# Kernel optimization log

Hardware: AMD Instinct MI355X
Metric: run time of the kernel (lower is better)

Reference implementation:

```python
import jax, jax.numpy as jnp
import numpy as np

NH = 16  # num_attention_heads
HD = 64  # attention_head_size (hidden 1024 / 16)

def _gelu(x):
    # matches torch.jit gelu: x * 0.5 * (1 + erf(x / 1.41421))
    return x * 0.5 * (1.0 + jax.lax.erf(x / 1.41421))

def setup_inputs() -> dict:
    key = jax.random.key(0)
    ks = jax.random.split(key, 6)
    B, S, H = 32, 512, 1024
    sc = 1.0 / np.sqrt(H)
    return {
        "hidden_states": jax.random.normal(ks[0], (B, S, H), jnp.float32),
        "Wq": jax.random.normal(ks[1], (H, H), jnp.float32) * sc,
        "bq": jnp.zeros((H,), jnp.float32),
        "Wk": jax.random.normal(ks[2], (H, H), jnp.float32) * sc,
        "bk": jnp.zeros((H,), jnp.float32),
        "Wv": jax.random.normal(ks[3], (H, H), jnp.float32) * sc,
        "bv": jnp.zeros((H,), jnp.float32),
        "Wp": jax.random.normal(ks[4], (3 * S, S), jnp.float32) * (1.0 / np.sqrt(3 * S)),
        "bp": jnp.zeros((S,), jnp.float32),
    }

def reference(hidden_states, Wq, bq, Wk, bk, Wv, bv, Wp, bp):
    b, s, h = hidden_states.shape
    # transpose_for_scores in the original is a pure .view (reshape), not a permute
    q = (hidden_states @ Wq + bq).reshape(b, NH, s, HD)
    k = (hidden_states @ Wk + bk).reshape(b, NH, s, HD)
    v = (hidden_states @ Wv + bv).reshape(b, NH, s, HD)
    # pooled global value: Linear over the (3*seq) axis, then gelu
    qkv = jnp.concatenate([q, k, v], axis=-2)              # (b, nh, 3s, hd)
    gv = jnp.swapaxes(qkv, -1, -2) @ Wp + bp               # (b, nh, hd, s)
    gv = _gelu(jnp.swapaxes(gv, -1, -2))                   # (b, nh, s, hd)
    # einsum('bnij,bnji->bni', q, k^T) == per-position dot product
    local = jnp.sum(q * k, axis=-1, keepdims=True)         # (b, nh, s, 1)
    scores = jnp.concatenate([local, jnp.zeros_like(local)], axis=-1)
    scores = scores / np.sqrt(HD)                          # (b, nh, s, 2)
    probs = jax.nn.softmax(scores, axis=-1)                # dropout prob = 0 (eval)
    v2 = jnp.stack([v, gv], axis=-2)                       # (b, nh, s, 2, hd)
    ctx = jnp.einsum('bnsk,bnskd->bnsd', probs, v2)        # (b, nh, s, hd)
    ctx = jnp.transpose(ctx, (0, 2, 1, 3)).reshape(b, s, NH * HD)
    return ctx
```

## Files before the change

### kernel.cpp

```cpp
#include <hip/hip_runtime.h>


typedef unsigned short ushort_t;
typedef __attribute__((ext_vector_type(8))) short short8;
typedef __attribute__((ext_vector_type(8))) unsigned short ushort8;
typedef __attribute__((ext_vector_type(4))) float f32x4;

#define ASYNC16(gp, lp) __builtin_amdgcn_global_load_lds( \
    (const __attribute__((address_space(1))) void*)(gp),  \
    (__attribute__((address_space(3))) void*)(lp), 16, 0, 0)

__device__ __forceinline__ ushort_t f2b(float f) {
  union { float f; unsigned int u; } v; v.f = f;
  unsigned int r = v.u + 0x7FFFu + ((v.u >> 16) & 1u);
  return (ushort_t)(r >> 16);
}
__device__ __forceinline__ float b2f(ushort_t b) {
  union { unsigned int u; float f; } v; v.u = ((unsigned int)b) << 16;
  return v.f;
}

#define OFF_HSB 0ull
#define OFF_WQT (33554432ull)
#define OFF_WKT (OFF_WQT + 2097152ull)
#define OFF_WVT (OFF_WKT + 2097152ull)
#define OFF_WPT (OFF_WVT + 2097152ull)
#define OFF_QF  (OFF_WPT + 1572864ull)
#define OFF_KF  (OFF_QF + 33554432ull)
#define OFF_VF  (OFF_KF + 33554432ull)

extern "C" __global__ __launch_bounds__(256) void k_cast(
    const float* __restrict__ src, ushort_t* __restrict__ dst) {
  int i = blockIdx.x * 256 + threadIdx.x;
  const float4* s = (const float4*)src + (size_t)i * 2;
  float4 a = s[0], b = s[1];
  ushort8 o;
  o[0] = f2b(a.x); o[1] = f2b(a.y); o[2] = f2b(a.z); o[3] = f2b(a.w);
  o[4] = f2b(b.x); o[5] = f2b(b.y); o[6] = f2b(b.z); o[7] = f2b(b.w);
  *((ushort8*)dst + i) = o;
}

extern "C" __global__ __launch_bounds__(256) void k_wt(
    const float* __restrict__ s0, const float* __restrict__ s1,
    const float* __restrict__ s2, const float* __restrict__ s3,
    ushort_t* __restrict__ d0, ushort_t* __restrict__ d1,
    ushort_t* __restrict__ d2, ushort_t* __restrict__ d3) {
  int z = blockIdx.z;
  const float* src = (z == 0) ? s0 : (z == 1) ? s1 : (z == 2) ? s2 : s3;
  ushort_t* dst    = (z == 0) ? d0 : (z == 1) ? d1 : (z == 2) ? d2 : d3;
  int R = (z == 3) ? 1536 : 1024;
  int C = (z == 3) ? 512  : 1024;
  int c0 = blockIdx.x * 64, r0 = blockIdx.y * 64;
  if (c0 >= C || r0 >= R) return;
  __shared__ ushort_t tl[64][80];
  int t = threadIdx.x;
  {
    int lr = t >> 2, cg = (t & 3) * 16;
    const float* sp = src + (size_t)(r0 + lr) * C + c0 + cg;
    #pragma unroll
    for (int i = 0; i < 16; ++i) tl[lr][cg + i] = f2b(sp[i]);
  }
  __syncthreads();
  {
    int lc = t >> 2, rg = (t & 3) * 16;
    ushort_t* dp = dst + (size_t)(c0 + lc) * R + r0 + rg;
    #pragma unroll
    for (int i = 0; i < 16; ++i) dp[i] = tl[rg + i][lc];
  }
}

extern "C" __global__ __launch_bounds__(256) void k_qkv(
    const ushort_t* __restrict__ A,
    const ushort_t* __restrict__ WTq, const ushort_t* __restrict__ WTk, const ushort_t* __restrict__ WTv,
    const float* __restrict__ bq, const float* __restrict__ bk, const float* __restrict__ bv,
    ushort_t* __restrict__ Qf, ushort_t* __restrict__ Kf, ushort_t* __restrict__ Vf) {
  int z = blockIdx.z;
  const ushort_t* WT = (z == 0) ? WTq : (z == 1) ? WTk : WTv;
  const float* bias  = (z == 0) ? bq  : (z == 1) ? bk  : bv;
  ushort_t* out      = (z == 0) ? Qf  : (z == 1) ? Kf  : Vf;

  int glin = blockIdx.y * 8 + blockIdx.x;
  int nl = (glin & 7) * 128 + (glin >> 3);
  int n0 = (nl & 7) * 128, m0 = (nl >> 3) * 128;

  __shared__ ushort_t lA[128 * 32];
  __shared__ ushort_t lB[128 * 32];
  int t = threadIdx.x, lane = t & 63, wave = t >> 6;
  int wr = (wave >> 1) * 64, wc = (wave & 1) * 64;

  f32x4 acc[4][4];
  #pragma unroll
  for (int mi = 0; mi < 4; ++mi)
    #pragma unroll
    for (int ni = 0; ni < 4; ++ni)
      acc[mi][ni] = (f32x4){0.f, 0.f, 0.f, 0.f};

  for (int k0 = 0; k0 < 1024; k0 += 32) {
    #pragma unroll
    for (int j = 0; j < 2; ++j) {
      int u = j * 256 + t;
      ASYNC16(A + (size_t)(m0 + (u >> 2)) * 1024 + k0 + (u & 3) * 8,
              (char*)lA + (j * 256 + wave * 64) * 16);
    }
    #pragma unroll
    for (int j = 0; j < 2; ++j) {
      int u = j * 256 + t;
      ASYNC16(WT + (size_t)(n0 + (u >> 2)) * 1024 + k0 + (u & 3) * 8,
              (char*)lB + (j * 256 + wave * 64) * 16);
    }
    __syncthreads();
    short8 af[4], bf[4];
    #pragma unroll
    for (int mi = 0; mi < 4; ++mi)
      af[mi] = *(const short8*)&lA[(wr + mi * 16 + (lane & 15)) * 32 + (lane >> 4) * 8];
    #pragma unroll
    for (int ni = 0; ni < 4; ++ni)
      bf[ni] = *(const short8*)&lB[(wc + ni * 16 + (lane & 15)) * 32 + (lane >> 4) * 8];
    #pragma unroll
    for (int mi = 0; mi < 4; ++mi)
      #pragma unroll
      for (int ni = 0; ni < 4; ++ni)
        acc[mi][ni] = __builtin_amdgcn_mfma_f32_16x16x32_bf16(af[mi], bf[ni], acc[mi][ni], 0, 0, 0);
    __syncthreads();
  }
  #pragma unroll
  for (int ni = 0; ni < 4; ++ni) {
    int gc = n0 + wc + ni * 16 + (lane & 15);
    float bv_ = bias[gc];
    #pragma unroll
    for (int mi = 0; mi < 4; ++mi) {
      int gr = m0 + wr + mi * 16 + ((lane >> 4) << 2);
      #pragma unroll
      for (int r = 0; r < 4; ++r)
        out[(size_t)(gr + r) * 1024 + gc] = f2b(acc[mi][ni][r] + bv_);
    }
  }
}

extern "C" __global__ __launch_bounds__(256) void k_tr(
    const ushort_t* __restrict__ src, ushort_t* __restrict__ dst) {
  int bn = blockIdx.x;
  const ushort_t* s = src + (size_t)bn * 32768;
  ushort_t* d = dst + (size_t)bn * 32768;
  __shared__ ushort_t tl[64][80];
  int t = threadIdx.x;
  for (int c = 0; c < 8; ++c) {
    #pragma unroll
    for (int j = 0; j < 2; ++j) {
      int u = j * 256 + t;
      int row = u >> 3, ch = (u & 7) * 8;
      uint4 v = *(const uint4*)&s[(size_t)(c * 64 + row) * 64 + ch];
      const ushort_t* pv = (const ushort_t*)&v;
      #pragma unroll
      for (int i = 0; i < 8; ++i) tl[ch + i][row] = pv[i];
    }
    __syncthreads();
    #pragma unroll
    for (int j = 0; j < 2; ++j) {
      int u = j * 256 + t;
      int dd = u >> 3, ch = (u & 7) * 8;
      *(uint4*)&d[(size_t)dd * 512 + c * 64 + ch] = *(const uint4*)&tl[dd][ch];
    }
    __syncthreads();
  }
}

extern "C" __global__ __launch_bounds__(256) void k_gv(
    const ushort_t* __restrict__ WpT,
    const ushort_t* __restrict__ QT, const ushort_t* __restrict__ KT, const ushort_t* __restrict__ VT,
    const float* __restrict__ bp, float* __restrict__ out) {
  int sh = blockIdx.x;
  int bn = blockIdx.y;
  int b = bn >> 4, nh = bn & 15;
  int s0 = sh * 256;
  int t = threadIdx.x, lane = t & 63, wave = t >> 6;

  __shared__ ushort_t lA[256 * 64];
  __shared__ ushort_t lB[64 * 64];
  __shared__ float p0s[256];

  const ushort_t* QTb = QT + (size_t)bn * 32768;
  const ushort_t* KTb = KT + (size_t)bn * 32768;
  const ushort_t* VTb = VT + (size_t)bn * 32768;

  {
    int s2 = s0 + t;
    float dot = 0.f;
    #pragma unroll 8
    for (int d = 0; d < 64; ++d)
      dot += b2f(QTb[(size_t)d * 512 + s2]) * b2f(KTb[(size_t)d * 512 + s2]);
    p0s[t] = 1.0f / (1.0f + __expf(-dot * 0.125f));
  }

  f32x4 acc[4][4];
  #pragma unroll
  for (int mi = 0; mi < 4; ++mi)
    #pragma unroll
    for (int ni = 0; ni < 4; ++ni)
      acc[mi][ni] = (f32x4){0.f, 0.f, 0.f, 0.f};

  for (int kt = 0; kt < 24; ++kt) {
    int t0 = kt * 64;
    const ushort_t* XT = (t0 < 512) ? QTb : (t0 < 1024) ? KTb : VTb;
    int t0l = t0 & 511;
    #pragma unroll
    for (int j = 0; j < 8; ++j) {
      int u = j * 256 + t;
      ASYNC16(WpT + (size_t)(s0 + (u >> 3)) * 1536 + t0 + (u & 7) * 8,
              (char*)lA + (j * 256 + wave * 64) * 16);
    }
    #pragma unroll
    for (int j = 0; j < 2; ++j) {
      int u = j * 256 + t;
      ASYNC16(XT + (size_t)(u >> 3) * 512 + t0l + (u & 7) * 8,
              (char*)lB + (j * 256 + wave * 64) * 16);
    }
    __syncthreads();
    #pragma unroll
    for (int kk = 0; kk < 2; ++kk) {
      short8 af[4], bf[4];
      #pragma unroll
      for (int mi = 0; mi < 4; ++mi)
        af[mi] = *(const short8*)&lA[(wave * 64 + mi * 16 + (lane & 15)) * 64 + kk * 32 + (lane >> 4) * 8];
      #pragma unroll
      for (int ni = 0; ni < 4; ++ni)
        bf[ni] = *(const short8*)&lB[(ni * 16 + (lane & 15)) * 64 + kk * 32 + (lane >> 4) * 8];
      #pragma unroll
      for (int mi = 0; mi < 4; ++mi)
        #pragma unroll
        for (int ni = 0; ni < 4; ++ni)
          acc[mi][ni] = __builtin_amdgcn_mfma_f32_16x16x32_bf16(af[mi], bf[ni], acc[mi][ni], 0, 0, 0);
    }
    __syncthreads();
  }

  size_t outb = (size_t)b * 512 * 1024 + (size_t)nh * 64;
  #pragma unroll
  for (int mi = 0; mi < 4; ++mi) {
    int sl = wave * 64 + mi * 16 + ((lane >> 4) << 2);
    #pragma unroll
    for (int r = 0; r < 4; ++r) {
      int s2 = s0 + sl + r;
      float p0 = p0s[sl + r];
      float bpv = bp[s2];
      #pragma unroll
      for (int ni = 0; ni < 4; ++ni) {
        int d = ni * 16 + (lane & 15);
        float g = acc[mi][ni][r] + bpv;
        float ge = 0.5f * g * (1.0f + erff(g / 1.41421f));
        float v = b2f(VTb[(size_t)d * 512 + s2]);
        out[outb + (size_t)s2 * 1024 + d] = p0 * v + (1.0f - p0) * ge;
      }
    }
  }
}

extern "C" void kernel_launch(void* const* d_in, const int* in_sizes, int n_in,
                              void* d_out, int out_size, void* d_ws, size_t ws_size,
                              hipStream_t stream) {
  const float* hs = (const float*)d_in[0];
  const float* Wq = (const float*)d_in[1];
  const float* bq = (const float*)d_in[2];
  const float* Wk = (const float*)d_in[3];
  const float* bk = (const float*)d_in[4];
  const float* Wv = (const float*)d_in[5];
  const float* bv = (const float*)d_in[6];
  const float* Wp = (const float*)d_in[7];
  const float* bp = (const float*)d_in[8];

  char* w = (char*)d_ws;
  ushort_t* hsb = (ushort_t*)(w + OFF_HSB);
  ushort_t* WqT = (ushort_t*)(w + OFF_WQT);
  ushort_t* WkT = (ushort_t*)(w + OFF_WKT);
  ushort_t* WvT = (ushort_t*)(w + OFF_WVT);
  ushort_t* WpT = (ushort_t*)(w + OFF_WPT);
  ushort_t* Qf  = (ushort_t*)(w + OFF_QF);
  ushort_t* Kf  = (ushort_t*)(w + OFF_KF);
  ushort_t* Vf  = (ushort_t*)(w + OFF_VF);
  ushort_t* QTt = (ushort_t*)(w + OFF_HSB);
  ushort_t* KTt = (ushort_t*)(w + OFF_QF);
  ushort_t* VTt = (ushort_t*)(w + OFF_KF);

  k_cast<<<8192, 256, 0, stream>>>(hs, hsb);
  k_wt<<<dim3(16, 24, 4), 256, 0, stream>>>(Wq, Wk, Wv, Wp, WqT, WkT, WvT, WpT);
  k_qkv<<<dim3(8, 128, 3), 256, 0, stream>>>(hsb, WqT, WkT, WvT, bq, bk, bv, Qf, Kf, Vf);
  k_tr<<<512, 256, 0, stream>>>(Qf, QTt);
  k_tr<<<512, 256, 0, stream>>>(Kf, KTt);
  k_tr<<<512, 256, 0, stream>>>(Vf, VTt);
  k_gv<<<dim3(2, 512), 256, 0, stream>>>(WpT, QTt, KTt, VTt, bp, (float*)d_out);
}
```

Baseline: 413.1 us.

## Share Wp tile across two batch-heads per block in k_gv

Each k_gv block now handles two (batch, head) pairs, so each Wp tile loaded into LDS feeds both. Waves split by head and by a 128-row half, and each wave accumulates 8x4 MFMA tiles instead of 4x4. This halves the Wp global traffic per output and puts blockIdx.x on the batch-head so neighbouring blocks share Wp. The local q·k dot also switches to vectorized 4-wide loads. The cost is more accumulator registers (launch bounds set to 2 blocks per SM), more LDS and half as many blocks.

```diff
diff --git a/kernel.cpp b/kernel.cpp
--- a/kernel.cpp
+++ b/kernel.cpp
@@ -165,83 +165,98 @@
   }
 }
 
-extern "C" __global__ __launch_bounds__(256) void k_gv(
+extern "C" __global__ __launch_bounds__(256, 2) void k_gv(
     const ushort_t* __restrict__ WpT,
     const ushort_t* __restrict__ QT, const ushort_t* __restrict__ KT, const ushort_t* __restrict__ VT,
     const float* __restrict__ bp, float* __restrict__ out) {
-  int sh = blockIdx.x;
-  int bn = blockIdx.y;
-  int b = bn >> 4, nh = bn & 15;
+  int bng = blockIdx.x;
+  int sh  = blockIdx.y;
   int s0 = sh * 256;
+  int bn0 = bng * 2;
   int t = threadIdx.x, lane = t & 63, wave = t >> 6;
+  int wbn = wave & 1;
+  int wr  = (wave >> 1) * 128;
 
   __shared__ ushort_t lA[256 * 64];
-  __shared__ ushort_t lB[64 * 64];
-  __shared__ float p0s[256];
-
-  const ushort_t* QTb = QT + (size_t)bn * 32768;
-  const ushort_t* KTb = KT + (size_t)bn * 32768;
-  const ushort_t* VTb = VT + (size_t)bn * 32768;
-
-  {
-    int s2 = s0 + t;
-    float dot = 0.f;
+  __shared__ ushort_t lB[2 * 64 * 64];
+  __shared__ float p0s[2][256];
+
+  if (t < 128) {
+    int bnl = t >> 6, qi = t & 63;
+    const ushort_t* Qb = QT + (size_t)(bn0 + bnl) * 32768 + s0 + qi * 4;
+    const ushort_t* Kb = KT + (size_t)(bn0 + bnl) * 32768 + s0 + qi * 4;
+    float dd0 = 0.f, dd1 = 0.f, dd2 = 0.f, dd3 = 0.f;
     #pragma unroll 8
-    for (int d = 0; d < 64; ++d)
-      dot += b2f(QTb[(size_t)d * 512 + s2]) * b2f(KTb[(size_t)d * 512 + s2]);
-    p0s[t] = 1.0f / (1.0f + __expf(-dot * 0.125f));
-  }
-
-  f32x4 acc[4][4];
+    for (int d = 0; d < 64; ++d) {
+      uint2 qv = *(const uint2*)(Qb + (size_t)d * 512);
+      uint2 kv = *(const uint2*)(Kb + (size_t)d * 512);
+      dd0 += b2f(qv.x & 0xffff) * b2f(kv.x & 0xffff);
+      dd1 += b2f(qv.x >> 16)    * b2f(kv.x >> 16);
+      dd2 += b2f(qv.y & 0xffff) * b2f(kv.y & 0xffff);
+      dd3 += b2f(qv.y >> 16)    * b2f(kv.y >> 16);
+    }
+    p0s[bnl][qi * 4 + 0] = 1.0f / (1.0f + __expf(-dd0 * 0.125f));
+    p0s[bnl][qi * 4 + 1] = 1.0f / (1.0f + __expf(-dd1 * 0.125f));
+    p0s[bnl][qi * 4 + 2] = 1.0f / (1.0f + __expf(-dd2 * 0.125f));
+    p0s[bnl][qi * 4 + 3] = 1.0f / (1.0f + __expf(-dd3 * 0.125f));
+  }
+
+  f32x4 acc[8][4];
   #pragma unroll
-  for (int mi = 0; mi < 4; ++mi)
+  for (int mi = 0; mi < 8; ++mi)
     #pragma unroll
     for (int ni = 0; ni < 4; ++ni)
       acc[mi][ni] = (f32x4){0.f, 0.f, 0.f, 0.f};
 
   for (int kt = 0; kt < 24; ++kt) {
     int t0 = kt * 64;
-    const ushort_t* XT = (t0 < 512) ? QTb : (t0 < 1024) ? KTb : VTb;
+    const ushort_t* XT = (t0 < 512) ? QT : (t0 < 1024) ? KT : VT;
     int t0l = t0 & 511;
     #pragma unroll
     for (int j = 0; j < 8; ++j) {
-      int u = j * 256 + t;
-      ASYNC16(WpT + (size_t)(s0 + (u >> 3)) * 1536 + t0 + (u & 7) * 8,
+      int uu = j * 256 + t;
+      ASYNC16(WpT + (size_t)(s0 + (uu >> 3)) * 1536 + t0 + (uu & 7) * 8,
               (char*)lA + (j * 256 + wave * 64) * 16);
     }
     #pragma unroll
-    for (int j = 0; j < 2; ++j) {
-      int u = j * 256 + t;
-      ASYNC16(XT + (size_t)(u >> 3) * 512 + t0l + (u & 7) * 8,
-              (char*)lB + (j * 256 + wave * 64) * 16);
+    for (int bl = 0; bl < 2; ++bl) {
+      const ushort_t* Xb = XT + (size_t)(bn0 + bl) * 32768;
+      #pragma unroll
+      for (int j = 0; j < 2; ++j) {
+        int uu = j * 256 + t;
+        ASYNC16(Xb + (size_t)(uu >> 3) * 512 + t0l + (uu & 7) * 8,
+                (char*)lB + bl * 8192 + (j * 256 + wave * 64) * 16);
+      }
     }
     __syncthreads();
     #pragma unroll
     for (int kk = 0; kk < 2; ++kk) {
-      short8 af[4], bf[4];
-      #pragma unroll
-      for (int mi = 0; mi < 4; ++mi)
-        af[mi] = *(const short8*)&lA[(wave * 64 + mi * 16 + (lane & 15)) * 64 + kk * 32 + (lane >> 4) * 8];
+      short8 bf[4];
       #pragma unroll
       for (int ni = 0; ni < 4; ++ni)
-        bf[ni] = *(const short8*)&lB[(ni * 16 + (lane & 15)) * 64 + kk * 32 + (lane >> 4) * 8];
-      #pragma unroll
-      for (int mi = 0; mi < 4; ++mi)
+        bf[ni] = *(const short8*)&lB[wbn * 4096 + (ni * 16 + (lane & 15)) * 64 + kk * 32 + (lane >> 4) * 8];
+      #pragma unroll
+      for (int mi = 0; mi < 8; ++mi) {
+        short8 af = *(const short8*)&lA[(wr + mi * 16 + (lane & 15)) * 64 + kk * 32 + (lane >> 4) * 8];
         #pragma unroll
         for (int ni = 0; ni < 4; ++ni)
-          acc[mi][ni] = __builtin_amdgcn_mfma_f32_16x16x32_bf16(af[mi], bf[ni], acc[mi][ni], 0, 0, 0);
-    }
-    __syncthreads();
-  }
-
+          acc[mi][ni] = __builtin_amdgcn_mfma_f32_16x16x32_bf16(af, bf[ni], acc[mi][ni], 0, 0, 0);
+      }
+    }
+    __syncthreads();
+  }
+
+  int bn = bn0 + wbn;
+  int b = bn >> 4, nh = bn & 15;
+  const ushort_t* VTb = VT + (size_t)bn * 32768;
   size_t outb = (size_t)b * 512 * 1024 + (size_t)nh * 64;
   #pragma unroll
-  for (int mi = 0; mi < 4; ++mi) {
-    int sl = wave * 64 + mi * 16 + ((lane >> 4) << 2);
+  for (int mi = 0; mi < 8; ++mi) {
+    int sl = wr + mi * 16 + ((lane >> 4) << 2);
     #pragma unroll
     for (int r = 0; r < 4; ++r) {
       int s2 = s0 + sl + r;
-      float p0 = p0s[sl + r];
+      float p0 = p0s[wbn][sl + r];
       float bpv = bp[s2];
       #pragma unroll
       for (int ni = 0; ni < 4; ++ni) {
@@ -287,5 +302,5 @@
   k_tr<<<512, 256, 0, stream>>>(Qf, QTt);
   k_tr<<<512, 256, 0, stream>>>(Kf, KTt);
   k_tr<<<512, 256, 0, stream>>>(Vf, VTt);
-  k_gv<<<dim3(2, 512), 256, 0, stream>>>(WpT, QTt, KTt, VTt, bp, (float*)d_out);
-}
+  k_gv<<<dim3(256, 2), 256, 0, stream>>>(WpT, QTt, KTt, VTt, bp, (float*)d_out);
+}
```

After: 416.8 us. No clear change (+0.9%).

## Recast pooled-value projection as one large GEMM with 128x128 tiles and split p0

Applied to the files above, without the earlier changes.

The per-(batch,head) gv kernel is replaced by a single large GEMM that treats all (b,nh,d) rows as M and sequence positions as N, using 128x128 tiles with a swizzled block order for L2 reuse of Wp. The sigmoid gate p0 is computed by a separate small kernel into workspace and read in the epilogue, and outputs are written as float4. This aims to raise tile reuse and remove the redundant per-block dot-product prologue, at the cost of an extra launch and a smaller K step (32) with more barriers.

```diff
diff --git a/kernel.cpp b/kernel.cpp
--- a/kernel.cpp
+++ b/kernel.cpp
@@ -165,32 +165,37 @@
   }
 }
 
-extern "C" __global__ __launch_bounds__(256) void k_gv(
-    const ushort_t* __restrict__ WpT,
-    const ushort_t* __restrict__ QT, const ushort_t* __restrict__ KT, const ushort_t* __restrict__ VT,
-    const float* __restrict__ bp, float* __restrict__ out) {
-  int sh = blockIdx.x;
-  int bn = blockIdx.y;
-  int b = bn >> 4, nh = bn & 15;
-  int s0 = sh * 256;
-  int t = threadIdx.x, lane = t & 63, wave = t >> 6;
-
-  __shared__ ushort_t lA[256 * 64];
-  __shared__ ushort_t lB[64 * 64];
-  __shared__ float p0s[256];
-
-  const ushort_t* QTb = QT + (size_t)bn * 32768;
-  const ushort_t* KTb = KT + (size_t)bn * 32768;
-  const ushort_t* VTb = VT + (size_t)bn * 32768;
-
-  {
-    int s2 = s0 + t;
+extern "C" __global__ __launch_bounds__(256) void k_p0(
+    const ushort_t* __restrict__ QT, const ushort_t* __restrict__ KT,
+    float* __restrict__ p0buf) {
+  int bn = blockIdx.x;
+  int t = threadIdx.x;
+  const ushort_t* Qb = QT + (size_t)bn * 32768;
+  const ushort_t* Kb = KT + (size_t)bn * 32768;
+  #pragma unroll
+  for (int sc = 0; sc < 2; ++sc) {
+    int s = sc * 256 + t;
     float dot = 0.f;
     #pragma unroll 8
     for (int d = 0; d < 64; ++d)
-      dot += b2f(QTb[(size_t)d * 512 + s2]) * b2f(KTb[(size_t)d * 512 + s2]);
-    p0s[t] = 1.0f / (1.0f + __expf(-dot * 0.125f));
-  }
+      dot += b2f(Qb[d * 512 + s]) * b2f(Kb[d * 512 + s]);
+    p0buf[bn * 512 + s] = 1.0f / (1.0f + __expf(-dot * 0.125f));
+  }
+}
+
+extern "C" __global__ __launch_bounds__(256) void k_gv2(
+    const ushort_t* __restrict__ QT, const ushort_t* __restrict__ KT, const ushort_t* __restrict__ VT,
+    const ushort_t* __restrict__ WpT, const float* __restrict__ p0buf,
+    const float* __restrict__ bp, float* __restrict__ out) {
+  int glin = blockIdx.y * 8 + blockIdx.x;
+  int nl = (glin & 7) * 128 + (glin >> 3);
+  int mt = nl >> 2, nt = nl & 3;
+  int m0 = mt * 128, n0 = nt * 128;
+
+  __shared__ ushort_t lA[128 * 32];
+  __shared__ ushort_t lB[128 * 32];
+  int t = threadIdx.x, lane = t & 63, wave = t >> 6;
+  int wr = (wave >> 1) * 64, wc = (wave & 1) * 64;
 
   f32x4 acc[4][4];
   #pragma unroll
@@ -199,58 +204,62 @@
     for (int ni = 0; ni < 4; ++ni)
       acc[mi][ni] = (f32x4){0.f, 0.f, 0.f, 0.f};
 
-  for (int kt = 0; kt < 24; ++kt) {
-    int t0 = kt * 64;
-    const ushort_t* XT = (t0 < 512) ? QTb : (t0 < 1024) ? KTb : VTb;
-    int t0l = t0 & 511;
-    #pragma unroll
-    for (int j = 0; j < 8; ++j) {
-      int u = j * 256 + t;
-      ASYNC16(WpT + (size_t)(s0 + (u >> 3)) * 1536 + t0 + (u & 7) * 8,
-              (char*)lA + (j * 256 + wave * 64) * 16);
-    }
-    #pragma unroll
-    for (int j = 0; j < 2; ++j) {
-      int u = j * 256 + t;
-      ASYNC16(XT + (size_t)(u >> 3) * 512 + t0l + (u & 7) * 8,
-              (char*)lB + (j * 256 + wave * 64) * 16);
-    }
-    __syncthreads();
-    #pragma unroll
-    for (int kk = 0; kk < 2; ++kk) {
+  for (int seg = 0; seg < 3; ++seg) {
+    const ushort_t* XT = (seg == 0) ? QT : (seg == 1) ? KT : VT;
+    for (int kk = 0; kk < 512; kk += 32) {
+      int k0 = seg * 512 + kk;
+      #pragma unroll
+      for (int j = 0; j < 2; ++j) {
+        int u = j * 256 + t;
+        int ar = m0 + (u >> 2);
+        ASYNC16(XT + ((size_t)(ar >> 6) << 15) + (size_t)(ar & 63) * 512 + kk + (u & 3) * 8,
+                (char*)lA + (j * 256 + wave * 64) * 16);
+      }
+      #pragma unroll
+      for (int j = 0; j < 2; ++j) {
+        int u = j * 256 + t;
+        ASYNC16(WpT + (size_t)(n0 + (u >> 2)) * 1536 + k0 + (u & 3) * 8,
+                (char*)lB + (j * 256 + wave * 64) * 16);
+      }
+      __syncthreads();
       short8 af[4], bf[4];
       #pragma unroll
       for (int mi = 0; mi < 4; ++mi)
-        af[mi] = *(const short8*)&lA[(wave * 64 + mi * 16 + (lane & 15)) * 64 + kk * 32 + (lane >> 4) * 8];
+        af[mi] = *(const short8*)&lA[(wr + mi * 16 + (lane & 15)) * 32 + (lane >> 4) * 8];
       #pragma unroll
       for (int ni = 0; ni < 4; ++ni)
-        bf[ni] = *(const short8*)&lB[(ni * 16 + (lane & 15)) * 64 + kk * 32 + (lane >> 4) * 8];
+        bf[ni] = *(const short8*)&lB[(wc + ni * 16 + (lane & 15)) * 32 + (lane >> 4) * 8];
       #pragma unroll
       for (int mi = 0; mi < 4; ++mi)
         #pragma unroll
         for (int ni = 0; ni < 4; ++ni)
           acc[mi][ni] = __builtin_amdgcn_mfma_f32_16x16x32_bf16(af[mi], bf[ni], acc[mi][ni], 0, 0, 0);
-    }
-    __syncthreads();
-  }
-
-  size_t outb = (size_t)b * 512 * 1024 + (size_t)nh * 64;
+      __syncthreads();
+    }
+  }
+
   #pragma unroll
   for (int mi = 0; mi < 4; ++mi) {
-    int sl = wave * 64 + mi * 16 + ((lane >> 4) << 2);
-    #pragma unroll
-    for (int r = 0; r < 4; ++r) {
-      int s2 = s0 + sl + r;
-      float p0 = p0s[sl + r];
-      float bpv = bp[s2];
-      #pragma unroll
-      for (int ni = 0; ni < 4; ++ni) {
-        int d = ni * 16 + (lane & 15);
+    int r0 = m0 + wr + mi * 16 + ((lane >> 4) << 2);
+    int bn = r0 >> 6, d0 = r0 & 63;
+    int b = bn >> 4, nh = bn & 15;
+    const ushort_t* VTb = VT + ((size_t)bn << 15);
+    const float* p0row = p0buf + bn * 512;
+    size_t outb = (size_t)b * 524288 + (size_t)nh * 64 + d0;
+    #pragma unroll
+    for (int ni = 0; ni < 4; ++ni) {
+      int gc = n0 + wc + ni * 16 + (lane & 15);
+      float p0 = p0row[gc];
+      float bpv = bp[gc];
+      float4 o;
+      #pragma unroll
+      for (int r = 0; r < 4; ++r) {
         float g = acc[mi][ni][r] + bpv;
         float ge = 0.5f * g * (1.0f + erff(g / 1.41421f));
-        float v = b2f(VTb[(size_t)d * 512 + s2]);
-        out[outb + (size_t)s2 * 1024 + d] = p0 * v + (1.0f - p0) * ge;
+        float v = b2f(VTb[(size_t)(d0 + r) * 512 + gc]);
+        ((float*)&o)[r] = p0 * v + (1.0f - p0) * ge;
       }
+      *(float4*)&out[outb + (size_t)gc * 1024] = o;
     }
   }
 }
@@ -280,6 +289,7 @@
   ushort_t* QTt = (ushort_t*)(w + OFF_HSB);
   ushort_t* KTt = (ushort_t*)(w + OFF_QF);
   ushort_t* VTt = (ushort_t*)(w + OFF_KF);
+  float*    p0b = (float*)(w + OFF_VF);
 
   k_cast<<<8192, 256, 0, stream>>>(hs, hsb);
   k_wt<<<dim3(16, 24, 4), 256, 0, stream>>>(Wq, Wk, Wv, Wp, WqT, WkT, WvT, WpT);
@@ -287,5 +297,6 @@
   k_tr<<<512, 256, 0, stream>>>(Qf, QTt);
   k_tr<<<512, 256, 0, stream>>>(Kf, KTt);
   k_tr<<<512, 256, 0, stream>>>(Vf, VTt);
-  k_gv<<<dim3(2, 512), 256, 0, stream>>>(WpT, QTt, KTt, VTt, bp, (float*)d_out);
-}
+  k_p0<<<512, 256, 0, stream>>>(QTt, KTt, p0b);
+  k_gv2<<<dim3(8, 128), 256, 0, stream>>>(QTt, KTt, VTt, WpT, p0b, bp, (float*)d_out);
+}
```

Result: faster. 402.6 us (-2.5%).
